# Optimization experiments

Measured on AMD Instinct MI355X. Metric: run time of the kernel, lower is better.

## Reference

```python
import jax, jax.numpy as jnp
import numpy as np

B = 4           # batchsize == poolsize, pool = arange(B)
N_NODES = 32768
N_EDGES = 262144
CH_V = 16
CH_E = 16
HID = 64
CH_MSG = 2 * CH_V + CH_E  # 48


def setup_inputs() -> dict:
    key = jax.random.key(0)
    ks = jax.random.split(key, 8)
    node_vals = jax.random.normal(ks[0], (B, N_NODES, CH_V), jnp.float32) * 0.01
    edge_vals = jax.random.normal(ks[1], (B, N_EDGES, CH_E), jnp.float32) * 0.1
    conn_a = jax.random.randint(ks[2], (N_EDGES,), 0, N_NODES)
    conn_b = jax.random.randint(ks[3], (N_EDGES,), 0, N_NODES)
    w = lambda k, sh: jax.random.normal(k, sh, jnp.float32) * 0.1
    return {
        "node_vals": node_vals, "edge_vals": edge_vals,
        "conn_a": conn_a, "conn_b": conn_b,
        "Wm1": w(ks[4], (CH_MSG, HID)), "bm1": jnp.zeros((HID,), jnp.float32),
        "Wm2": w(ks[5], (HID, CH_MSG)), "bm2": jnp.zeros((CH_MSG,), jnp.float32),
        "Wu1": w(ks[6], (3 * CH_V, HID)), "bu1": jnp.zeros((HID,), jnp.float32),
        "Wu2": w(ks[7], (HID, CH_V)), "bu2": jnp.zeros((CH_V,), jnp.float32),
    }


def reference(node_vals, edge_vals, conn_a, conn_b,
              Wm1, bm1, Wm2, bm2, Wu1, bu1, Wu2, bu2):
    # NeuralGraph.timestep with node_dropout_p = edge_dropout_p = 0 (masks are identity),
    # use_update=True, average_messages=True, nodes=True, edges=True.
    h_a = node_vals[:, conn_a]                      # [B, E, CH_V] gather at source nodes
    h_b = node_vals[:, conn_b]                      # [B, E, CH_V] gather at target nodes
    h = jnp.concatenate([h_a, h_b, edge_vals], -1)  # [B, E, 48]
    # message MLP (Linear -> tanh -> Linear)
    m = jnp.tanh(h @ Wm1 + bm1) @ Wm2 + bm2         # [B, E, 48]
    m_a = m[..., :CH_V]
    m_b = m[..., CH_V:2 * CH_V]
    m_ab = m[..., 2 * CH_V:]
    # scatter-add aggregation per node (index_add_ along node dim)
    agg_a = jnp.zeros((B, N_NODES, CH_V), m.dtype).at[:, conn_a].add(m_a)
    agg_b = jnp.zeros((B, N_NODES, CH_V), m.dtype).at[:, conn_b].add(m_b)
    # count-based averaging (counts clamped to >= 1, matching the buffer fixup)
    ones = jnp.ones((N_EDGES,), m.dtype)
    cnt_a = jnp.maximum(jax.ops.segment_sum(ones, conn_a, num_segments=N_NODES), 1.0)
    cnt_b = jnp.maximum(jax.ops.segment_sum(ones, conn_b, num_segments=N_NODES), 1.0)
    agg_a = agg_a / cnt_a[None, :, None]
    agg_b = agg_b / cnt_b[None, :, None]
    # update MLP
    u_in = jnp.concatenate([agg_a, agg_b, node_vals], -1)   # [B, N, 48]
    updates = jnp.tanh(u_in @ Wu1 + bu1) @ Wu2 + bu2        # [B, N, CH_V]
    new_node_vals = node_vals + updates
    new_edge_vals = edge_vals + m_ab
    return new_node_vals, new_edge_vals
```

## Files before the change

kernel.cpp:

```cpp
#include <hip/hip_runtime.h>
#include <hip/hip_bf16.h>
#include <cstdint>
#include <cstddef>

#define B 4
#define NN 32768
#define NE 262144
#define CV 16
#define CE 16
#define HID 64
#define CM 48

using frag  = __attribute__((ext_vector_type(8))) short;
using f32x4 = __attribute__((ext_vector_type(4))) float;

__device__ __forceinline__ float fast_tanh(float x) {
    float e = __expf(2.0f * x);
    return 1.0f - 2.0f / (e + 1.0f);
}

__device__ __forceinline__ unsigned short f2bf(float x) {
    union { float f; unsigned u; } v; v.f = x;
    unsigned r = (v.u + 0x7FFFu + ((v.u >> 16) & 1u)) >> 16;
    return (unsigned short)r;
}

__device__ __forceinline__ float bf2f(unsigned short x) {
    union { unsigned u; float f; } v; v.u = ((unsigned)x) << 16;
    return v.f;
}

__device__ __forceinline__ unsigned pk2bf(float lo, float hi) {
    union { __hip_bfloat162 h; unsigned u; } v;
    v.h = __float22bfloat162_rn(make_float2(lo, hi));
    return v.u;
}

__device__ __forceinline__ unsigned swo(int row, int byte_off) {
    return (unsigned)((row << 7) + (byte_off ^ ((row & 7) << 4)));
}

__device__ __forceinline__ void acc8(float* a, uint4 v) {
    a[0] += bf2f((unsigned short)(v.x & 0xFFFFu));
    a[1] += bf2f((unsigned short)(v.x >> 16));
    a[2] += bf2f((unsigned short)(v.y & 0xFFFFu));
    a[3] += bf2f((unsigned short)(v.y >> 16));
    a[4] += bf2f((unsigned short)(v.z & 0xFFFFu));
    a[5] += bf2f((unsigned short)(v.z >> 16));
    a[6] += bf2f((unsigned short)(v.w & 0xFFFFu));
    a[7] += bf2f((unsigned short)(v.w >> 16));
}

__global__ __launch_bounds__(256) void count_kernel(
    const int* __restrict__ ca, const int* __restrict__ cb,
    int* __restrict__ cnt_a, int* __restrict__ cnt_b,
    int* __restrict__ rank_a, int* __restrict__ rank_b,
    const float* __restrict__ Wm1, const float* __restrict__ bm1,
    const float* __restrict__ Wm2,
    const float* __restrict__ Wu1, const float* __restrict__ bu1,
    const float* __restrict__ Wu2,
    const float* __restrict__ node_vals,
    unsigned short* __restrict__ pW1, unsigned short* __restrict__ pW2,
    unsigned short* __restrict__ pWu1, unsigned short* __restrict__ pWu2,
    unsigned short* __restrict__ nv16)
{
    int i = blockIdx.x * 256 + threadIdx.x;
    rank_a[i] = atomicAdd(&cnt_a[ca[i]], 1);
    rank_b[i] = atomicAdd(&cnt_b[cb[i]], 1);

    {
        int x0 = i * 8;
        const float4* src = (const float4*)(node_vals + x0);
        float4 v0 = src[0], v1 = src[1];
        uint4 o;
        o.x = pk2bf(v0.x, v0.y); o.y = pk2bf(v0.z, v0.w);
        o.z = pk2bf(v1.x, v1.y); o.w = pk2bf(v1.z, v1.w);
        *(uint4*)(nv16 + x0) = o;
    }

    if (blockIdx.x == 0) {
        for (int x = threadIdx.x; x < 4 * 2 * 64 * 8; x += 256) {
            int j = x & 7, lane = (x >> 3) & 63, ks = (x >> 9) & 1, mt = x >> 10;
            int m = mt * 16 + (lane & 15);
            int k = ks * 32 + (lane >> 4) * 8 + j;
            float w = (k < 48) ? Wm1[k * 64 + m] : (k == 48 ? bm1[m] : 0.0f);
            pW1[x] = f2bf(w);
        }
    } else if (blockIdx.x == 1) {
        for (int x = threadIdx.x; x < 3 * 2 * 64 * 8; x += 256) {
            int j = x & 7, lane = (x >> 3) & 63, ks = (x >> 9) & 1, mt = x >> 10;
            int m = mt * 16 + (lane & 15);
            int k = ks * 32 + (lane >> 4) * 8 + j;
            pW2[x] = f2bf(Wm2[k * 48 + m]);
        }
    } else if (blockIdx.x == 2) {
        for (int x = threadIdx.x; x < 4 * 2 * 64 * 8; x += 256) {
            int j = x & 7, lane = (x >> 3) & 63, ks = (x >> 9) & 1, mt = x >> 10;
            int m = mt * 16 + (lane & 15);
            int k = ks * 32 + (lane >> 4) * 8 + j;
            float w = (k < 48) ? Wu1[k * 64 + m] : (k == 48 ? bu1[m] : 0.0f);
            pWu1[x] = f2bf(w);
        }
    } else if (blockIdx.x == 3) {
        for (int x = threadIdx.x; x < 2 * 64 * 8; x += 256) {
            int j = x & 7, lane = (x >> 3) & 63, ks = x >> 9;
            int m = lane & 15;
            int k = ks * 32 + (lane >> 4) * 8 + j;
            pWu2[x] = f2bf(Wu2[k * 16 + m]);
        }
    }
}

__global__ __launch_bounds__(1024) void scan_kernel(
    const int* __restrict__ cnt_a, int* __restrict__ start_a,
    const int* __restrict__ cnt_b, int* __restrict__ start_b)
{
    const int* cnt = (blockIdx.x == 0) ? cnt_a : cnt_b;
    int* start     = (blockIdx.x == 0) ? start_a : start_b;

    __shared__ int sw[16];
    int t = threadIdx.x;
    int lane = t & 63;
    int wv   = t >> 6;
    int base = t * 32;

    int local[32];
    int sum = 0;
    const int4* p = (const int4*)(cnt + base);
#pragma unroll
    for (int q = 0; q < 8; q++) {
        int4 v = p[q];
        local[q*4+0] = v.x; local[q*4+1] = v.y; local[q*4+2] = v.z; local[q*4+3] = v.w;
        sum += v.x + v.y + v.z + v.w;
    }
    int inc = sum;
#pragma unroll
    for (int off = 1; off < 64; off <<= 1) {
        int u = __shfl_up(inc, off);
        if (lane >= off) inc += u;
    }
    if (lane == 63) sw[wv] = inc;
    __syncthreads();
    if (wv == 0 && lane < 16) {
        int v = sw[lane];
        int i2 = v;
#pragma unroll
        for (int off = 1; off < 16; off <<= 1) {
            int u = __shfl_up(i2, off);
            if (lane >= off) i2 += u;
        }
        sw[lane] = i2 - v;
    }
    __syncthreads();

    int run = sw[wv] + inc - sum;
    int4* ps = (int4*)(start + base);
#pragma unroll
    for (int q = 0; q < 8; q++) {
        int4 o;
        o.x = run; run += local[q*4+0];
        o.y = run; run += local[q*4+1];
        o.z = run; run += local[q*4+2];
        o.w = run; run += local[q*4+3];
        ps[q] = o;
    }
}

__global__ __launch_bounds__(256) void eidx_kernel(
    const int* __restrict__ ca, const int* __restrict__ cb,
    const int* __restrict__ rank_a, const int* __restrict__ rank_b,
    const int* __restrict__ start_a, const int* __restrict__ start_b,
    int* __restrict__ eidx_a, int* __restrict__ eidx_b)
{
    int e = blockIdx.x * 256 + threadIdx.x;
    eidx_a[start_a[ca[e]] + rank_a[e]] = e;
    eidx_b[start_b[cb[e]] + rank_b[e]] = e;
}

__global__ __launch_bounds__(256, 5) void edge_kernel(
    const unsigned short* __restrict__ nv16, const float* __restrict__ edge_vals,
    const int* __restrict__ ca, const int* __restrict__ cb,
    const unsigned short* __restrict__ pW1, const unsigned short* __restrict__ pW2,
    const float* __restrict__ bm2,
    float* __restrict__ out_edge,
    unsigned short* __restrict__ ma, unsigned short* __restrict__ mb)
{
    __shared__ unsigned short sH[256 * 64];
    char* sB = (char*)sH;

    int t    = threadIdx.x;
    int lane = t & 63;
    int col  = lane & 15;
    int quad = lane >> 4;
    int erow = (t >> 6) * 64;
    int cha  = quad * 4;

    size_t eb  = (size_t)blockIdx.x * 256;
    size_t idx = eb + t;
    int e  = (int)(idx & (NE - 1));
    int bb = (int)(idx >> 18);

    int na = ca[e], nb = cb[e];

    {
        const uint4* gA = (const uint4*)(nv16 + ((size_t)bb * NN + na) * CV);
        const uint4* gB = (const uint4*)(nv16 + ((size_t)bb * NN + nb) * CV);
        uint4 a0 = gA[0], a1 = gA[1];
        uint4 b0 = gB[0], b1 = gB[1];
        const float4* pE = (const float4*)(edge_vals + idx * CE);
        float4 ev0 = pE[0], ev1 = pE[1], ev2 = pE[2], ev3 = pE[3];

        unsigned pk[32];
        *(uint4*)&pk[0]  = a0;  *(uint4*)&pk[4]  = a1;
        *(uint4*)&pk[8]  = b0;  *(uint4*)&pk[12] = b1;
        pk[16] = pk2bf(ev0.x, ev0.y); pk[17] = pk2bf(ev0.z, ev0.w);
        pk[18] = pk2bf(ev1.x, ev1.y); pk[19] = pk2bf(ev1.z, ev1.w);
        pk[20] = pk2bf(ev2.x, ev2.y); pk[21] = pk2bf(ev2.z, ev2.w);
        pk[22] = pk2bf(ev3.x, ev3.y); pk[23] = pk2bf(ev3.z, ev3.w);
        pk[24] = 0x3F80u;
#pragma unroll
        for (int q = 25; q < 32; q++) pk[q] = 0;
        const uint4* src = (const uint4*)pk;
#pragma unroll
        for (int q = 0; q < 8; q++)
            *(uint4*)(sB + swo(t, q * 16)) = src[q];
    }
    asm volatile("s_waitcnt lgkmcnt(0)" ::: "memory");

#pragma unroll
    for (int hh = 0; hh < 2; hh++) {
        int r0 = erow + hh * 32 + col;

        frag w1f[4][2];
#pragma unroll
        for (int mt = 0; mt < 4; mt++)
#pragma unroll
            for (int ks = 0; ks < 2; ks++)
                w1f[mt][ks] = *(const frag*)&pW1[(((mt * 2 + ks) * 64) + lane) * 8];

        f32x4 acc1[4][2];
#pragma unroll
        for (int mt = 0; mt < 4; mt++)
#pragma unroll
            for (int n = 0; n < 2; n++) acc1[mt][n] = (f32x4){0.f, 0.f, 0.f, 0.f};

#pragma unroll
        for (int ks = 0; ks < 2; ks++) {
            frag bfr[2];
#pragma unroll
            for (int n = 0; n < 2; n++)
                bfr[n] = *(const frag*)(sB + swo(r0 + n * 16, ks * 64 + quad * 16));
#pragma unroll
            for (int mt = 0; mt < 4; mt++)
#pragma unroll
                for (int n = 0; n < 2; n++)
                    acc1[mt][n] = __builtin_amdgcn_mfma_f32_16x16x32_bf16(
                        w1f[mt][ks], bfr[n], acc1[mt][n], 0, 0, 0);
        }

#pragma unroll
        for (int n = 0; n < 2; n++) {
            int row = r0 + n * 16;
#pragma unroll
            for (int mt = 0; mt < 4; mt++) {
                uint2 w;
                w.x = pk2bf(fast_tanh(acc1[mt][n][0]), fast_tanh(acc1[mt][n][1]));
                w.y = pk2bf(fast_tanh(acc1[mt][n][2]), fast_tanh(acc1[mt][n][3]));
                *(uint2*)(sB + swo(row, mt * 32 + quad * 8)) = w;
            }
        }
        asm volatile("s_waitcnt lgkmcnt(0)" ::: "memory");

        frag w2f[3][2];
#pragma unroll
        for (int mt = 0; mt < 3; mt++)
#pragma unroll
            for (int ks = 0; ks < 2; ks++)
                w2f[mt][ks] = *(const frag*)&pW2[(((mt * 2 + ks) * 64) + lane) * 8];

        f32x4 acc2[3][2];
#pragma unroll
        for (int mt = 0; mt < 3; mt++)
#pragma unroll
            for (int n = 0; n < 2; n++) acc2[mt][n] = (f32x4){0.f, 0.f, 0.f, 0.f};

#pragma unroll
        for (int ks = 0; ks < 2; ks++) {
            frag bfr[2];
#pragma unroll
            for (int n = 0; n < 2; n++)
                bfr[n] = *(const frag*)(sB + swo(r0 + n * 16, ks * 64 + quad * 16));
#pragma unroll
            for (int mt = 0; mt < 3; mt++)
#pragma unroll
                for (int n = 0; n < 2; n++)
                    acc2[mt][n] = __builtin_amdgcn_mfma_f32_16x16x32_bf16(
                        w2f[mt][ks], bfr[n], acc2[mt][n], 0, 0, 0);
        }

        float4 b2e = *(const float4*)&bm2[32 + cha];
#pragma unroll
        for (int n = 0; n < 2; n++) {
            int le = r0 + n * 16;
            size_t o = (eb + le) * CE + cha;
            float4 evv = *(const float4*)&edge_vals[o];
            float4 ov;
            ov.x = evv.x + acc2[2][n][0] + b2e.x;
            ov.y = evv.y + acc2[2][n][1] + b2e.y;
            ov.z = evv.z + acc2[2][n][2] + b2e.z;
            ov.w = evv.w + acc2[2][n][3] + b2e.w;
            *(float4*)&out_edge[o] = ov;
        }

        float4 b2a = *(const float4*)&bm2[cha];
        float4 b2b = *(const float4*)&bm2[16 + cha];
#pragma unroll
        for (int n = 0; n < 2; n++) {
            int row = r0 + n * 16;
            uint2 wa;
            wa.x = pk2bf(acc2[0][n][0] + b2a.x, acc2[0][n][1] + b2a.y);
            wa.y = pk2bf(acc2[0][n][2] + b2a.z, acc2[0][n][3] + b2a.w);
            *(uint2*)(sB + swo(row, quad * 8)) = wa;
            uint2 wb;
            wb.x = pk2bf(acc2[1][n][0] + b2b.x, acc2[1][n][1] + b2b.y);
            wb.y = pk2bf(acc2[1][n][2] + b2b.z, acc2[1][n][3] + b2b.w);
            *(uint2*)(sB + swo(row, 32 + quad * 8)) = wb;
        }
    }
    asm volatile("s_waitcnt lgkmcnt(0)" ::: "memory");

    {
        uint4 a0 = *(const uint4*)(sB + swo(t, 0));
        uint4 a1 = *(const uint4*)(sB + swo(t, 16));
        uint4 b0 = *(const uint4*)(sB + swo(t, 32));
        uint4 b1 = *(const uint4*)(sB + swo(t, 48));
        unsigned short* pa = &ma[idx * 16];
        *(uint4*)(pa + 0) = a0;
        *(uint4*)(pa + 8) = a1;
        unsigned short* pb = &mb[idx * 16];
        *(uint4*)(pb + 0) = b0;
        *(uint4*)(pb + 8) = b1;
    }
}

__global__ __launch_bounds__(256) void node_kernel(
    const float* __restrict__ node_vals,
    const unsigned short* __restrict__ ma, const unsigned short* __restrict__ mb,
    const int* __restrict__ eidx_a, const int* __restrict__ eidx_b,
    const int* __restrict__ start_a, const int* __restrict__ start_b,
    const int* __restrict__ cnt_a, const int* __restrict__ cnt_b,
    const unsigned short* __restrict__ pWu1, const unsigned short* __restrict__ pWu2,
    const float* __restrict__ bu2,
    float* __restrict__ out_node)
{
    __shared__ unsigned short sH[256 * 64];
    char* sB = (char*)sH;

    int t    = threadIdx.x;
    int lane = t & 63;
    int col  = lane & 15;
    int quad = lane >> 4;
    int erow = (t >> 6) * 64;

    int g = blockIdx.x * 256 + t;
    int n = g & (NN - 1);
    int b = g >> 15;

    float4 pn[4];
    {
        float ua[16] = {0.f,0.f,0.f,0.f,0.f,0.f,0.f,0.f,0.f,0.f,0.f,0.f,0.f,0.f,0.f,0.f};
        float ub[16] = {0.f,0.f,0.f,0.f,0.f,0.f,0.f,0.f,0.f,0.f,0.f,0.f,0.f,0.f,0.f,0.f};
        int da = cnt_a[n], sa = start_a[n];
        int db = cnt_b[n], sbn = start_b[n];
        const int* ia = eidx_a + sa;
        const int* ib = eidx_b + sbn;
        const unsigned short* mab = ma + (size_t)b * NE * 16;
        const unsigned short* mbb = mb + (size_t)b * NE * 16;
        for (int k = 0; k < da; k++) {
            int ee = ia[k];
            const uint4* p = (const uint4*)(mab + (size_t)ee * 16);
            acc8(&ua[0], p[0]);
            acc8(&ua[8], p[1]);
        }
        for (int k = 0; k < db; k++) {
            int ee = ib[k];
            const uint4* p = (const uint4*)(mbb + (size_t)ee * 16);
            acc8(&ub[0], p[0]);
            acc8(&ub[8], p[1]);
        }
        float inva = 1.0f / (float)max(da, 1);
        float invb = 1.0f / (float)max(db, 1);

        const float4* pnv = (const float4*)(node_vals + (size_t)g * CV);
#pragma unroll
        for (int q = 0; q < 4; q++) pn[q] = pnv[q];

        unsigned pk[32];
#pragma unroll
        for (int q = 0; q < 8; q++)
            pk[q] = pk2bf(ua[2*q] * inva, ua[2*q+1] * inva);
#pragma unroll
        for (int q = 0; q < 8; q++)
            pk[8 + q] = pk2bf(ub[2*q] * invb, ub[2*q+1] * invb);
#pragma unroll
        for (int q = 0; q < 4; q++) {
            pk[16 + 2*q + 0] = pk2bf(pn[q].x, pn[q].y);
            pk[16 + 2*q + 1] = pk2bf(pn[q].z, pn[q].w);
        }
        pk[24] = 0x3F80u;
#pragma unroll
        for (int q = 25; q < 32; q++) pk[q] = 0;
        const uint4* src = (const uint4*)pk;
#pragma unroll
        for (int q = 0; q < 8; q++)
            *(uint4*)(sB + swo(t, q * 16)) = src[q];
    }
    asm volatile("s_waitcnt lgkmcnt(0)" ::: "memory");

    frag w1f[4][2];
#pragma unroll
    for (int mt = 0; mt < 4; mt++)
#pragma unroll
        for (int ks = 0; ks < 2; ks++)
            w1f[mt][ks] = *(const frag*)&pWu1[(((mt * 2 + ks) * 64) + lane) * 8];

    f32x4 acc1[4][4];
#pragma unroll
    for (int mt = 0; mt < 4; mt++)
#pragma unroll
        for (int nt = 0; nt < 4; nt++) acc1[mt][nt] = (f32x4){0.f, 0.f, 0.f, 0.f};

#pragma unroll
    for (int ks = 0; ks < 2; ks++) {
        frag bfr[4];
#pragma unroll
        for (int nt = 0; nt < 4; nt++)
            bfr[nt] = *(const frag*)(sB + swo(erow + nt*16 + col, ks * 64 + quad * 16));
#pragma unroll
        for (int mt = 0; mt < 4; mt++)
#pragma unroll
            for (int nt = 0; nt < 4; nt++)
                acc1[mt][nt] = __builtin_amdgcn_mfma_f32_16x16x32_bf16(
                    w1f[mt][ks], bfr[nt], acc1[mt][nt], 0, 0, 0);
    }

#pragma unroll
    for (int nt = 0; nt < 4; nt++) {
        int row = erow + nt*16 + col;
#pragma unroll
        for (int mt = 0; mt < 4; mt++) {
            uint2 w;
            w.x = pk2bf(fast_tanh(acc1[mt][nt][0]), fast_tanh(acc1[mt][nt][1]));
            w.y = pk2bf(fast_tanh(acc1[mt][nt][2]), fast_tanh(acc1[mt][nt][3]));
            *(uint2*)(sB + swo(row, mt * 32 + quad * 8)) = w;
        }
    }
    asm volatile("s_waitcnt lgkmcnt(0)" ::: "memory");

    frag w2f[2];
#pragma unroll
    for (int ks = 0; ks < 2; ks++)
        w2f[ks] = *(const frag*)&pWu2[(ks * 64 + lane) * 8];

    f32x4 acc2[4];
#pragma unroll
    for (int nt = 0; nt < 4; nt++) acc2[nt] = (f32x4){0.f, 0.f, 0.f, 0.f};

#pragma unroll
    for (int ks = 0; ks < 2; ks++) {
        frag bfr[4];
#pragma unroll
        for (int nt = 0; nt < 4; nt++)
            bfr[nt] = *(const frag*)(sB + swo(erow + nt*16 + col, ks * 64 + quad * 16));
#pragma unroll
        for (int nt = 0; nt < 4; nt++)
            acc2[nt] = __builtin_amdgcn_mfma_f32_16x16x32_bf16(
                w2f[ks], bfr[nt], acc2[nt], 0, 0, 0);
    }

#pragma unroll
    for (int nt = 0; nt < 4; nt++) {
        int row = erow + nt*16 + col;
        float4 v;
        v.x = acc2[nt][0]; v.y = acc2[nt][1];
        v.z = acc2[nt][2]; v.w = acc2[nt][3];
        *(float4*)(sB + swo(row, quad * 16)) = v;
    }
    asm volatile("s_waitcnt lgkmcnt(0)" ::: "memory");

    {
        const float4* pb2 = (const float4*)bu2;
        float4* po = (float4*)&out_node[(size_t)g * CV];
#pragma unroll
        for (int q = 0; q < 4; q++) {
            float4 m = *(const float4*)(sB + swo(t, q * 16));
            float4 c = pb2[q];
            float4 o;
            o.x = pn[q].x + m.x + c.x;
            o.y = pn[q].y + m.y + c.y;
            o.z = pn[q].z + m.z + c.z;
            o.w = pn[q].w + m.w + c.w;
            po[q] = o;
        }
    }
}

extern "C" void kernel_launch(void* const* d_in, const int* in_sizes, int n_in,
                              void* d_out, int out_size, void* d_ws, size_t ws_size,
                              hipStream_t stream) {
    const float* node_vals = (const float*)d_in[0];
    const float* edge_vals = (const float*)d_in[1];
    const int*   ca        = (const int*)d_in[2];
    const int*   cb        = (const int*)d_in[3];
    const float* Wm1 = (const float*)d_in[4];
    const float* bm1 = (const float*)d_in[5];
    const float* Wm2 = (const float*)d_in[6];
    const float* bm2 = (const float*)d_in[7];
    const float* Wu1 = (const float*)d_in[8];
    const float* bu1 = (const float*)d_in[9];
    const float* Wu2 = (const float*)d_in[10];
    const float* bu2 = (const float*)d_in[11];

    float* out_node = (float*)d_out;
    float* out_edge = out_node + (size_t)B * NN * CV;

    unsigned short* ma = (unsigned short*)d_ws;
    unsigned short* mb = ma + (size_t)B * NE * 16;
    int* cnt_a   = (int*)(mb + (size_t)B * NE * 16);
    int* cnt_b   = cnt_a + NN;
    int* start_a = cnt_b + NN;
    int* start_b = start_a + NN;
    int* rank_a  = start_b + NN;
    int* rank_b  = rank_a + NE;
    int* eidx_a  = rank_b + NE;
    int* eidx_b  = eidx_a + NE;
    unsigned short* pW1  = (unsigned short*)(eidx_b + NE);
    unsigned short* pW2  = pW1 + 4096;
    unsigned short* pWu1 = pW2 + 3072;
    unsigned short* pWu2 = pWu1 + 4096;
    unsigned short* nv16 = pWu2 + 1024;

    hipMemsetAsync(cnt_a, 0, 2 * (size_t)NN * sizeof(int), stream);

    count_kernel<<<NE / 256, 256, 0, stream>>>(
        ca, cb, cnt_a, cnt_b, rank_a, rank_b,
        Wm1, bm1, Wm2, Wu1, bu1, Wu2, node_vals,
        pW1, pW2, pWu1, pWu2, nv16);
    scan_kernel<<<2, 1024, 0, stream>>>(cnt_a, start_a, cnt_b, start_b);
    eidx_kernel<<<NE / 256, 256, 0, stream>>>(
        ca, cb, rank_a, rank_b, start_a, start_b, eidx_a, eidx_b);
    edge_kernel<<<(B * NE) / 256, 256, 0, stream>>>(
        nv16, edge_vals, ca, cb, pW1, pW2, bm2, out_edge, ma, mb);
    node_kernel<<<(B * NN) / 256, 256, 0, stream>>>(
        node_vals, ma, mb, eidx_a, eidx_b, start_a, start_b, cnt_a, cnt_b,
        pWu1, pWu2, bu2, out_node);
}
```

Baseline: 282.8 us.

## Fuse degree counting into edge kernel and split node MLP into halves

The per-edge atomic degree counting and rank assignment move out of the prep kernel and into the edge kernel, done only by batch 0 threads, so the prep kernel no longer waits on atomics and the counting overlaps the edge MLP work. Scan and eidx now launch after the edge kernel. The node kernel processes its 64 rows per wave in two 32-row halves to shrink accumulator register pressure, and sets launch bounds to 4 blocks per SM. The layer-2 output is written to a separate LDS column region so it does not overwrite inputs still needed by the second half.

```diff
diff --git a/kernel.cpp b/kernel.cpp
--- a/kernel.cpp
+++ b/kernel.cpp
@@ -51,10 +51,7 @@
     a[7] += bf2f((unsigned short)(v.w >> 16));
 }
 
-__global__ __launch_bounds__(256) void count_kernel(
-    const int* __restrict__ ca, const int* __restrict__ cb,
-    int* __restrict__ cnt_a, int* __restrict__ cnt_b,
-    int* __restrict__ rank_a, int* __restrict__ rank_b,
+__global__ __launch_bounds__(256) void prep_kernel(
     const float* __restrict__ Wm1, const float* __restrict__ bm1,
     const float* __restrict__ Wm2,
     const float* __restrict__ Wu1, const float* __restrict__ bu1,
@@ -65,8 +62,6 @@
     unsigned short* __restrict__ nv16)
 {
     int i = blockIdx.x * 256 + threadIdx.x;
-    rank_a[i] = atomicAdd(&cnt_a[ca[i]], 1);
-    rank_b[i] = atomicAdd(&cnt_b[cb[i]], 1);
 
     {
         int x0 = i * 8;
@@ -180,6 +175,8 @@
 __global__ __launch_bounds__(256, 5) void edge_kernel(
     const unsigned short* __restrict__ nv16, const float* __restrict__ edge_vals,
     const int* __restrict__ ca, const int* __restrict__ cb,
+    int* __restrict__ cnt_a, int* __restrict__ cnt_b,
+    int* __restrict__ rank_a, int* __restrict__ rank_b,
     const unsigned short* __restrict__ pW1, const unsigned short* __restrict__ pW2,
     const float* __restrict__ bm2,
     float* __restrict__ out_edge,
@@ -201,6 +198,11 @@
     int bb = (int)(idx >> 18);
 
     int na = ca[e], nb = cb[e];
+
+    if (bb == 0) {
+        rank_a[e] = atomicAdd(&cnt_a[na], 1);
+        rank_b[e] = atomicAdd(&cnt_b[nb], 1);
+    }
 
     {
         const uint4* gA = (const uint4*)(nv16 + ((size_t)bb * NN + na) * CV);
@@ -343,7 +345,7 @@
     }
 }
 
-__global__ __launch_bounds__(256) void node_kernel(
+__global__ __launch_bounds__(256, 4) void node_kernel(
     const float* __restrict__ node_vals,
     const unsigned short* __restrict__ ma, const unsigned short* __restrict__ mb,
     const int* __restrict__ eidx_a, const int* __restrict__ eidx_b,
@@ -417,74 +419,79 @@
     }
     asm volatile("s_waitcnt lgkmcnt(0)" ::: "memory");
 
-    frag w1f[4][2];
-#pragma unroll
-    for (int mt = 0; mt < 4; mt++)
+#pragma unroll
+    for (int hh = 0; hh < 2; hh++) {
+        int r0 = erow + hh * 32 + col;
+
+        frag w1f[4][2];
+#pragma unroll
+        for (int mt = 0; mt < 4; mt++)
+#pragma unroll
+            for (int ks = 0; ks < 2; ks++)
+                w1f[mt][ks] = *(const frag*)&pWu1[(((mt * 2 + ks) * 64) + lane) * 8];
+
+        f32x4 acc1[4][2];
+#pragma unroll
+        for (int mt = 0; mt < 4; mt++)
+#pragma unroll
+            for (int nt = 0; nt < 2; nt++) acc1[mt][nt] = (f32x4){0.f, 0.f, 0.f, 0.f};
+
+#pragma unroll
+        for (int ks = 0; ks < 2; ks++) {
+            frag bfr[2];
+#pragma unroll
+            for (int nt = 0; nt < 2; nt++)
+                bfr[nt] = *(const frag*)(sB + swo(r0 + nt * 16, ks * 64 + quad * 16));
+#pragma unroll
+            for (int mt = 0; mt < 4; mt++)
+#pragma unroll
+                for (int nt = 0; nt < 2; nt++)
+                    acc1[mt][nt] = __builtin_amdgcn_mfma_f32_16x16x32_bf16(
+                        w1f[mt][ks], bfr[nt], acc1[mt][nt], 0, 0, 0);
+        }
+
+#pragma unroll
+        for (int nt = 0; nt < 2; nt++) {
+            int row = r0 + nt * 16;
+#pragma unroll
+            for (int mt = 0; mt < 4; mt++) {
+                uint2 w;
+                w.x = pk2bf(fast_tanh(acc1[mt][nt][0]), fast_tanh(acc1[mt][nt][1]));
+                w.y = pk2bf(fast_tanh(acc1[mt][nt][2]), fast_tanh(acc1[mt][nt][3]));
+                *(uint2*)(sB + swo(row, mt * 32 + quad * 8)) = w;
+            }
+        }
+        asm volatile("s_waitcnt lgkmcnt(0)" ::: "memory");
+
+        frag w2f[2];
 #pragma unroll
         for (int ks = 0; ks < 2; ks++)
-            w1f[mt][ks] = *(const frag*)&pWu1[(((mt * 2 + ks) * 64) + lane) * 8];
-
-    f32x4 acc1[4][4];
-#pragma unroll
-    for (int mt = 0; mt < 4; mt++)
-#pragma unroll
-        for (int nt = 0; nt < 4; nt++) acc1[mt][nt] = (f32x4){0.f, 0.f, 0.f, 0.f};
-
-#pragma unroll
-    for (int ks = 0; ks < 2; ks++) {
-        frag bfr[4];
-#pragma unroll
-        for (int nt = 0; nt < 4; nt++)
-            bfr[nt] = *(const frag*)(sB + swo(erow + nt*16 + col, ks * 64 + quad * 16));
-#pragma unroll
-        for (int mt = 0; mt < 4; mt++)
-#pragma unroll
-            for (int nt = 0; nt < 4; nt++)
-                acc1[mt][nt] = __builtin_amdgcn_mfma_f32_16x16x32_bf16(
-                    w1f[mt][ks], bfr[nt], acc1[mt][nt], 0, 0, 0);
-    }
-
-#pragma unroll
-    for (int nt = 0; nt < 4; nt++) {
-        int row = erow + nt*16 + col;
-#pragma unroll
-        for (int mt = 0; mt < 4; mt++) {
-            uint2 w;
-            w.x = pk2bf(fast_tanh(acc1[mt][nt][0]), fast_tanh(acc1[mt][nt][1]));
-            w.y = pk2bf(fast_tanh(acc1[mt][nt][2]), fast_tanh(acc1[mt][nt][3]));
-            *(uint2*)(sB + swo(row, mt * 32 + quad * 8)) = w;
-        }
-    }
-    asm volatile("s_waitcnt lgkmcnt(0)" ::: "memory");
-
-    frag w2f[2];
-#pragma unroll
-    for (int ks = 0; ks < 2; ks++)
-        w2f[ks] = *(const frag*)&pWu2[(ks * 64 + lane) * 8];
-
-    f32x4 acc2[4];
-#pragma unroll
-    for (int nt = 0; nt < 4; nt++) acc2[nt] = (f32x4){0.f, 0.f, 0.f, 0.f};
-
-#pragma unroll
-    for (int ks = 0; ks < 2; ks++) {
-        frag bfr[4];
-#pragma unroll
-        for (int nt = 0; nt < 4; nt++)
-            bfr[nt] = *(const frag*)(sB + swo(erow + nt*16 + col, ks * 64 + quad * 16));
-#pragma unroll
-        for (int nt = 0; nt < 4; nt++)
-            acc2[nt] = __builtin_amdgcn_mfma_f32_16x16x32_bf16(
-                w2f[ks], bfr[nt], acc2[nt], 0, 0, 0);
-    }
-
-#pragma unroll
-    for (int nt = 0; nt < 4; nt++) {
-        int row = erow + nt*16 + col;
-        float4 v;
-        v.x = acc2[nt][0]; v.y = acc2[nt][1];
-        v.z = acc2[nt][2]; v.w = acc2[nt][3];
-        *(float4*)(sB + swo(row, quad * 16)) = v;
+            w2f[ks] = *(const frag*)&pWu2[(ks * 64 + lane) * 8];
+
+        f32x4 acc2[2];
+#pragma unroll
+        for (int nt = 0; nt < 2; nt++) acc2[nt] = (f32x4){0.f, 0.f, 0.f, 0.f};
+
+#pragma unroll
+        for (int ks = 0; ks < 2; ks++) {
+            frag bfr[2];
+#pragma unroll
+            for (int nt = 0; nt < 2; nt++)
+                bfr[nt] = *(const frag*)(sB + swo(r0 + nt * 16, ks * 64 + quad * 16));
+#pragma unroll
+            for (int nt = 0; nt < 2; nt++)
+                acc2[nt] = __builtin_amdgcn_mfma_f32_16x16x32_bf16(
+                    w2f[ks], bfr[nt], acc2[nt], 0, 0, 0);
+        }
+
+#pragma unroll
+        for (int nt = 0; nt < 2; nt++) {
+            int row = r0 + nt * 16;
+            float4 v;
+            v.x = acc2[nt][0]; v.y = acc2[nt][1];
+            v.z = acc2[nt][2]; v.w = acc2[nt][3];
+            *(float4*)(sB + swo(row, 64 + quad * 16)) = v;
+        }
     }
     asm volatile("s_waitcnt lgkmcnt(0)" ::: "memory");
 
@@ -493,7 +500,7 @@
         float4* po = (float4*)&out_node[(size_t)g * CV];
 #pragma unroll
         for (int q = 0; q < 4; q++) {
-            float4 m = *(const float4*)(sB + swo(t, q * 16));
+            float4 m = *(const float4*)(sB + swo(t, 64 + q * 16));
             float4 c = pb2[q];
             float4 o;
             o.x = pn[q].x + m.x + c.x;
@@ -542,15 +549,15 @@
 
     hipMemsetAsync(cnt_a, 0, 2 * (size_t)NN * sizeof(int), stream);
 
-    count_kernel<<<NE / 256, 256, 0, stream>>>(
-        ca, cb, cnt_a, cnt_b, rank_a, rank_b,
+    prep_kernel<<<NE / 256, 256, 0, stream>>>(
         Wm1, bm1, Wm2, Wu1, bu1, Wu2, node_vals,
         pW1, pW2, pWu1, pWu2, nv16);
+    edge_kernel<<<(B * NE) / 256, 256, 0, stream>>>(
+        nv16, edge_vals, ca, cb, cnt_a, cnt_b, rank_a, rank_b,
+        pW1, pW2, bm2, out_edge, ma, mb);
     scan_kernel<<<2, 1024, 0, stream>>>(cnt_a, start_a, cnt_b, start_b);
     eidx_kernel<<<NE / 256, 256, 0, stream>>>(
         ca, cb, rank_a, rank_b, start_a, start_b, eidx_a, eidx_b);
-    edge_kernel<<<(B * NE) / 256, 256, 0, stream>>>(
-        nv16, edge_vals, ca, cb, pW1, pW2, bm2, out_edge, ma, mb);
     node_kernel<<<(B * NN) / 256, 256, 0, stream>>>(
         node_vals, ma, mb, eidx_a, eidx_b, start_a, start_b, cnt_a, cnt_b,
         pWu1, pWu2, bu2, out_node);
```

Measured after the change: 288.6 us. +2.1%, slower.
